# Optimization experiments

Hardware: AMD Instinct MI355X
Metric: run time of the kernel (lower is better)

Reference implementation:

```python
import jax, jax.numpy as jnp
from jax import lax
import numpy as np

B, T, IN, H, OUT = 8192, 512, 8, 64, 1


def setup_inputs() -> dict:
    key = jax.random.key(0)
    ks = jax.random.split(key, 7)
    s_ih = 1.0 / np.sqrt(H)
    # PyTorch LSTM param layout: gates stacked as [i, f, g, o] along dim 0
    W_ih = jax.random.uniform(ks[0], (4 * H, IN), jnp.float32, -s_ih, s_ih)
    W_hh = jax.random.uniform(ks[1], (4 * H, H), jnp.float32, -s_ih, s_ih)
    b_ih = jax.random.uniform(ks[2], (4 * H,), jnp.float32, -s_ih, s_ih)
    b_hh = jax.random.uniform(ks[3], (4 * H,), jnp.float32, -s_ih, s_ih)
    W_fc = jax.random.uniform(ks[4], (OUT, H), jnp.float32, -s_ih, s_ih)
    b_fc = jax.random.uniform(ks[5], (OUT,), jnp.float32, -s_ih, s_ih)
    x = jax.random.normal(ks[6], (B, T, IN), jnp.float32)
    return {"x": x, "W_ih": W_ih, "W_hh": W_hh, "b_ih": b_ih,
            "b_hh": b_hh, "W_fc": W_fc, "b_fc": b_fc}


def _lstm_last_h(x, W_ih, W_hh, b_ih, b_hh):
    # x: [B, T, IN] -> last hidden state [B, H]
    Bn = x.shape[0]
    Hn = W_hh.shape[1]
    b = b_ih + b_hh  # [4H]

    def step(carry, xt):
        h, c = carry  # [B, H] each
        gates = xt @ W_ih.T + h @ W_hh.T + b  # [B, 4H]
        i, f, g, o = jnp.split(gates, 4, axis=-1)
        i = jax.nn.sigmoid(i)
        f = jax.nn.sigmoid(f)
        g = jnp.tanh(g)
        o = jax.nn.sigmoid(o)
        c = f * c + i * g
        h = o * jnp.tanh(c)
        return (h, c), None

    h0 = jnp.zeros((Bn, Hn), x.dtype)
    c0 = jnp.zeros((Bn, Hn), x.dtype)
    (hT, _), _ = lax.scan(step, (h0, c0), jnp.swapaxes(x, 0, 1))  # scan over T
    return hT


def reference(x, W_ih, W_hh, b_ih, b_hh, W_fc, b_fc):
    hT = _lstm_last_h(x, W_ih, W_hh, b_ih, b_hh)  # [B, H]
    return hT @ W_fc.T + b_fc  # [B, OUT]
```

## Files before the change

kernel.cpp:

```cpp
#include <hip/hip_runtime.h>


typedef _Float16 f16_t;
typedef _Float16 half8 __attribute__((ext_vector_type(8)));
typedef _Float16 half4 __attribute__((ext_vector_type(4)));
typedef __fp16 fp16x2 __attribute__((ext_vector_type(2)));
typedef float floatx2 __attribute__((ext_vector_type(2)));
typedef float floatx4 __attribute__((ext_vector_type(4)));

#define Bn 8192
#define Tn 512
#define INn 8
#define Hn 64
#define BT 16
#define CHUNK 16
#define NCHUNK (Tn / CHUNK)
#define HSTRIDE 72
#define XROW 24

#define SOFT_BARRIER() asm volatile("s_waitcnt lgkmcnt(0)\n\ts_barrier" ::: "memory")

__device__ __forceinline__ floatx2 act_pair(float zi0, float zi1,
                                            float zf0, float zf1,
                                            float zg0, float zg1,
                                            float zo0, float zo1,
                                            floatx2& chat) {
  const floatx2 one  = {1.f, 1.f};
  const float  K2   = 2.8853900817779268f;
  const floatx2 K2v  = {K2, K2};
  const floatx2 mK2v = {-K2, -K2};
  const floatx2 clmp = {126.f, 126.f};
  floatx2 A = {__builtin_amdgcn_exp2f(zi0), __builtin_amdgcn_exp2f(zi1)};
  floatx2 G = {__builtin_amdgcn_exp2f(zg0), __builtin_amdgcn_exp2f(zg1)};
  floatx2 F = {__builtin_amdgcn_exp2f(zf0), __builtin_amdgcn_exp2f(zf1)};
  floatx2 O = {__builtin_amdgcn_exp2f(zo0), __builtin_amdgcn_exp2f(zo1)};
  floatx2 PA  = A + one;
  floatx2 PG  = G + one;
  floatx2 PF  = F + one;
  floatx2 PAG = PA * PG;
  floatx2 num = __builtin_elementwise_fma(G, K2v, mK2v) * PF;
  floatx2 s   = __builtin_elementwise_fma(chat, PAG, num);
  floatx2 P3  = PF * PAG;
  floatx2 R   = {__builtin_amdgcn_rcpf(P3.x), __builtin_amdgcn_rcpf(P3.y)};
  chat = __builtin_elementwise_min(s * R, clmp);
  floatx2 C2 = {__builtin_amdgcn_exp2f(chat.x), __builtin_amdgcn_exp2f(chat.y)};
  floatx2 P4 = (O + one) * (C2 + one);
  floatx2 Rh = {__builtin_amdgcn_rcpf(P4.x), __builtin_amdgcn_rcpf(P4.y)};
  return (C2 - one) * Rh;
}

__global__ __launch_bounds__(256, 2)
void lstm_fused(const float* __restrict__ xg,
                const float* __restrict__ W_ih,
                const float* __restrict__ W_hh,
                const float* __restrict__ b_ih,
                const float* __restrict__ b_hh,
                const float* __restrict__ W_fc,
                const float* __restrict__ b_fc,
                float* __restrict__ out)
{
  __shared__ alignas(16) f16_t hbuf[2][BT][HSTRIDE];
  __shared__ alignas(16) f16_t xlds[2][CHUNK][BT][XROW];

  const int tid   = threadIdx.x;
  const int wv    = tid >> 6;
  const int lane  = tid & 63;
  const int n     = lane & 15;
  const int q     = lane >> 4;
  const int bbase = blockIdx.x * BT;

  const float LOG2E = 1.4426950408889634f;

  half8 bf[4][2];
  half4 bfx[4];
  #pragma unroll
  for (int g = 0; g < 4; ++g) {
    const float sc = (g == 2) ? (2.f * LOG2E) : (-LOG2E);
    const int C = g * 64 + wv * 16 + n;
    #pragma unroll
    for (int c = 0; c < 2; ++c) {
      half8 v;
      #pragma unroll
      for (int j = 0; j < 8; ++j) {
        const int k = c * 32 + q * 8 + j;
        v[j] = (f16_t)(W_hh[C * Hn + k] * sc);
      }
      bf[g][c] = v;
    }
    half4 vx;
    #pragma unroll
    for (int j = 0; j < 4; ++j) {
      const int k = q * 4 + j;
      vx[j] = (f16_t)((k < INn) ? (W_ih[C * INn + k] * sc) : 0.f);
    }
    bfx[g] = vx;
  }

  const int u0 = wv * 16 + q * 4;
  floatx4 bi, bfv, bg, bo;
  #pragma unroll
  for (int r = 0; r < 4; ++r) {
    const int uu = u0 + r;
    bi[r]  = -(b_ih[uu]        + b_hh[uu])        * LOG2E;
    bfv[r] = -(b_ih[64 + uu]   + b_hh[64 + uu])   * LOG2E;
    bg[r]  =  (b_ih[128 + uu]  + b_hh[128 + uu])  * (2.f * LOG2E);
    bo[r]  = -(b_ih[192 + uu]  + b_hh[192 + uu])  * LOG2E;
  }

  const int row_s = tid >> 4;
  const int tt_s  = tid & 15;
  const float* xps = xg + ((size_t)(bbase + row_s) * Tn + tt_s) * INn;

  for (int i = tid; i < BT * HSTRIDE; i += 256) ((f16_t*)hbuf[0])[i] = (f16_t)0.f;
  {
    const half8 z = {};
    #pragma unroll
    for (int r = tid; r < 2 * CHUNK * BT; r += 256) {
      f16_t* base = &xlds[r >> 8][(r >> 4) & 15][r & 15][0];
      *(half8*)(base + 8)  = z;
      *(half8*)(base + 16) = z;
    }
  }
  {
    float4 a  = *(const float4*)(xps);
    float4 b2 = *(const float4*)(xps + 4);
    union { half8 v; fp16x2 h2[4]; } P;
    P.h2[0] = __builtin_amdgcn_cvt_pkrtz(a.x, a.y);
    P.h2[1] = __builtin_amdgcn_cvt_pkrtz(a.z, a.w);
    P.h2[2] = __builtin_amdgcn_cvt_pkrtz(b2.x, b2.y);
    P.h2[3] = __builtin_amdgcn_cvt_pkrtz(b2.z, b2.w);
    *(half8*)&xlds[0][tt_s][row_s][0] = P.v;
  }
  float4 pa  = *(const float4*)(xps + CHUNK * INn);
  float4 pb2 = *(const float4*)(xps + CHUNK * INn + 4);

  __syncthreads();

  if (blockIdx.x & 256) {
    #pragma unroll
    for (int sdel = 0; sdel < 6; ++sdel) __builtin_amdgcn_s_sleep(2);
  }

  floatx2 chat01 = {0.f, 0.f};
  floatx2 chat23 = {0.f, 0.f};

  for (int ch = 0; ch < NCHUNK; ++ch) {
    half4 bx[CHUNK];
    #pragma unroll
    for (int t = 0; t < CHUNK; ++t)
      bx[t] = *(const half4*)&xlds[ch & 1][t][n][q * 4];

    #pragma unroll
    for (int tt = 0; tt < CHUNK; ++tt) {
      const int p  = tt & 1;
      const int pn = p ^ 1;

      const half8 b0 = *(const half8*)&hbuf[p][n][q * 8];
      const half8 b1 = *(const half8*)&hbuf[p][n][32 + q * 8];

      __builtin_amdgcn_s_setprio(1);
      floatx4 ai = __builtin_amdgcn_mfma_f32_16x16x32_f16(bf[0][0], b0, bi,  0, 0, 0);
      floatx4 af = __builtin_amdgcn_mfma_f32_16x16x32_f16(bf[1][0], b0, bfv, 0, 0, 0);
      floatx4 ag = __builtin_amdgcn_mfma_f32_16x16x32_f16(bf[2][0], b0, bg,  0, 0, 0);
      floatx4 ao = __builtin_amdgcn_mfma_f32_16x16x32_f16(bf[3][0], b0, bo,  0, 0, 0);
      ai = __builtin_amdgcn_mfma_f32_16x16x32_f16(bf[0][1], b1, ai, 0, 0, 0);
      af = __builtin_amdgcn_mfma_f32_16x16x32_f16(bf[1][1], b1, af, 0, 0, 0);
      ag = __builtin_amdgcn_mfma_f32_16x16x32_f16(bf[2][1], b1, ag, 0, 0, 0);
      ao = __builtin_amdgcn_mfma_f32_16x16x32_f16(bf[3][1], b1, ao, 0, 0, 0);
      ai = __builtin_amdgcn_mfma_f32_16x16x16f16(bfx[0], bx[tt], ai, 0, 0, 0);
      af = __builtin_amdgcn_mfma_f32_16x16x16f16(bfx[1], bx[tt], af, 0, 0, 0);
      ag = __builtin_amdgcn_mfma_f32_16x16x16f16(bfx[2], bx[tt], ag, 0, 0, 0);
      ao = __builtin_amdgcn_mfma_f32_16x16x16f16(bfx[3], bx[tt], ao, 0, 0, 0);
      __builtin_amdgcn_s_setprio(0);

      if (tt == 0) {
        union { half8 v; fp16x2 h2[4]; } P;
        P.h2[0] = __builtin_amdgcn_cvt_pkrtz(pa.x, pa.y);
        P.h2[1] = __builtin_amdgcn_cvt_pkrtz(pa.z, pa.w);
        P.h2[2] = __builtin_amdgcn_cvt_pkrtz(pb2.x, pb2.y);
        P.h2[3] = __builtin_amdgcn_cvt_pkrtz(pb2.z, pb2.w);
        *(half8*)&xlds[(ch + 1) & 1][tt_s][row_s][0] = P.v;
      }
      if (tt == 1) {
        const int chn = (ch + 2 < NCHUNK) ? (ch + 2) : (ch + 2 - NCHUNK);
        pa  = *(const float4*)(xps + (size_t)chn * CHUNK * INn);
        pb2 = *(const float4*)(xps + (size_t)chn * CHUNK * INn + 4);
      }

      const floatx2 h01 = act_pair(ai[0], ai[1], af[0], af[1],
                                   ag[0], ag[1], ao[0], ao[1], chat01);
      const floatx2 h23 = act_pair(ai[2], ai[3], af[2], af[3],
                                   ag[2], ag[3], ao[2], ao[3], chat23);

      union { half4 v; fp16x2 h2[2]; } Wq;
      Wq.h2[0] = __builtin_amdgcn_cvt_pkrtz(h01.x, h01.y);
      Wq.h2[1] = __builtin_amdgcn_cvt_pkrtz(h23.x, h23.y);
      *(half4*)&hbuf[pn][n][u0] = Wq.v;

      SOFT_BARRIER();
    }
  }

  if (tid < 64) {
    const int b = lane & 15;
    const int part = lane >> 4;
    float s = 0.f;
    #pragma unroll
    for (int k = 0; k < 16; ++k) {
      const int uu = part * 16 + k;
      s = __builtin_fmaf((float)hbuf[0][b][uu], W_fc[uu], s);
    }
    s += __shfl_down(s, 32);
    s += __shfl_down(s, 16);
    if (lane < 16) out[bbase + b] = s + b_fc[0];
  }
}

extern "C" void kernel_launch(void* const* d_in, const int* in_sizes, int n_in,
                              void* d_out, int out_size, void* d_ws, size_t ws_size,
                              hipStream_t stream) {
  const float* x    = (const float*)d_in[0];
  const float* W_ih = (const float*)d_in[1];
  const float* W_hh = (const float*)d_in[2];
  const float* b_ih = (const float*)d_in[3];
  const float* b_hh = (const float*)d_in[4];
  const float* W_fc = (const float*)d_in[5];
  const float* b_fc = (const float*)d_in[6];
  float* out = (float*)d_out;
  dim3 grid(Bn / BT), block(256);
  hipLaunchKernelGGL(lstm_fused, grid, block, 0, stream,
                     x, W_ih, W_hh, b_ih, b_hh, W_fc, b_fc, out);
}
```

Measured before the change: 437.9 us.

## Interleave two batch tiles per block to overlap MFMA with activations

Each block now owns two 16-row batch tiles instead of one. Within each timestep it issues the gate MFMAs of one tile while computing the activations of the other, with a barrier after each half-step. This is meant to hide the dependent MFMA-to-activation latency explicitly rather than relying on two co-resident blocks per CU, so launch bounds drop to one block per CU and the grid is halved. The s_sleep stagger, setprio hints and per-chunk register caching of x are removed. In exchange there are twice as many barriers per block, extra LDS reads of x every step, and one wasted MFMA batch at the end of the loop.

```diff
diff --git a/kernel.cpp b/kernel.cpp
--- a/kernel.cpp
+++ b/kernel.cpp
@@ -13,6 +13,7 @@
 #define INn 8
 #define Hn 64
 #define BT 16
+#define NT 2
 #define CHUNK 16
 #define NCHUNK (Tn / CHUNK)
 #define HSTRIDE 72
@@ -49,7 +50,7 @@
   return (C2 - one) * Rh;
 }
 
-__global__ __launch_bounds__(256, 2)
+__global__ __launch_bounds__(256, 1)
 void lstm_fused(const float* __restrict__ xg,
                 const float* __restrict__ W_ih,
                 const float* __restrict__ W_hh,
@@ -59,15 +60,15 @@
                 const float* __restrict__ b_fc,
                 float* __restrict__ out)
 {
-  __shared__ alignas(16) f16_t hbuf[2][BT][HSTRIDE];
-  __shared__ alignas(16) f16_t xlds[2][CHUNK][BT][XROW];
+  __shared__ alignas(16) f16_t hbuf[NT][2][BT][HSTRIDE];
+  __shared__ alignas(16) f16_t xlds[NT][2][CHUNK][BT][XROW];
 
   const int tid   = threadIdx.x;
   const int wv    = tid >> 6;
   const int lane  = tid & 63;
   const int n     = lane & 15;
   const int q     = lane >> 4;
-  const int bbase = blockIdx.x * BT;
+  const int bbase = blockIdx.x * (BT * NT);
 
   const float LOG2E = 1.4426950408889634f;
 
@@ -109,110 +110,168 @@
 
   const int row_s = tid >> 4;
   const int tt_s  = tid & 15;
-  const float* xps = xg + ((size_t)(bbase + row_s) * Tn + tt_s) * INn;
-
-  for (int i = tid; i < BT * HSTRIDE; i += 256) ((f16_t*)hbuf[0])[i] = (f16_t)0.f;
+  const float* xps0 = xg + ((size_t)(bbase + row_s) * Tn + tt_s) * INn;
+  const float* xps1 = xps0 + (size_t)BT * Tn * INn;
+
+  for (int i = tid; i < NT * 2 * BT * HSTRIDE; i += 256)
+    ((f16_t*)hbuf)[i] = (f16_t)0.f;
   {
     const half8 z = {};
-    #pragma unroll
-    for (int r = tid; r < 2 * CHUNK * BT; r += 256) {
-      f16_t* base = &xlds[r >> 8][(r >> 4) & 15][r & 15][0];
+    for (int r = tid; r < NT * 2 * CHUNK * BT; r += 256) {
+      f16_t* base = ((f16_t*)xlds) + (size_t)r * XROW;
       *(half8*)(base + 8)  = z;
       *(half8*)(base + 16) = z;
     }
   }
   {
-    float4 a  = *(const float4*)(xps);
-    float4 b2 = *(const float4*)(xps + 4);
+    float4 a  = *(const float4*)(xps0);
+    float4 b2 = *(const float4*)(xps0 + 4);
     union { half8 v; fp16x2 h2[4]; } P;
     P.h2[0] = __builtin_amdgcn_cvt_pkrtz(a.x, a.y);
     P.h2[1] = __builtin_amdgcn_cvt_pkrtz(a.z, a.w);
     P.h2[2] = __builtin_amdgcn_cvt_pkrtz(b2.x, b2.y);
     P.h2[3] = __builtin_amdgcn_cvt_pkrtz(b2.z, b2.w);
-    *(half8*)&xlds[0][tt_s][row_s][0] = P.v;
-  }
-  float4 pa  = *(const float4*)(xps + CHUNK * INn);
-  float4 pb2 = *(const float4*)(xps + CHUNK * INn + 4);
+    *(half8*)&xlds[0][0][tt_s][row_s][0] = P.v;
+    a  = *(const float4*)(xps1);
+    b2 = *(const float4*)(xps1 + 4);
+    P.h2[0] = __builtin_amdgcn_cvt_pkrtz(a.x, a.y);
+    P.h2[1] = __builtin_amdgcn_cvt_pkrtz(a.z, a.w);
+    P.h2[2] = __builtin_amdgcn_cvt_pkrtz(b2.x, b2.y);
+    P.h2[3] = __builtin_amdgcn_cvt_pkrtz(b2.z, b2.w);
+    *(half8*)&xlds[1][0][tt_s][row_s][0] = P.v;
+  }
+  float4 pa0 = *(const float4*)(xps0 + CHUNK * INn);
+  float4 pb0 = *(const float4*)(xps0 + CHUNK * INn + 4);
+  float4 pa1 = *(const float4*)(xps1 + CHUNK * INn);
+  float4 pb1 = *(const float4*)(xps1 + CHUNK * INn + 4);
 
   __syncthreads();
 
-  if (blockIdx.x & 256) {
-    #pragma unroll
-    for (int sdel = 0; sdel < 6; ++sdel) __builtin_amdgcn_s_sleep(2);
-  }
-
-  floatx2 chat01 = {0.f, 0.f};
-  floatx2 chat23 = {0.f, 0.f};
+  floatx2 chat0_01 = {0.f, 0.f}, chat0_23 = {0.f, 0.f};
+  floatx2 chat1_01 = {0.f, 0.f}, chat1_23 = {0.f, 0.f};
+
+  floatx4 t0i, t0f, t0g, t0o;
+  {
+    const half8 d0 = *(const half8*)&hbuf[0][0][n][q * 8];
+    const half8 d1 = *(const half8*)&hbuf[0][0][n][32 + q * 8];
+    const half4 bx0 = *(const half4*)&xlds[0][0][0][n][q * 4];
+    t0i = __builtin_amdgcn_mfma_f32_16x16x32_f16(bf[0][0], d0, bi,  0, 0, 0);
+    t0f = __builtin_amdgcn_mfma_f32_16x16x32_f16(bf[1][0], d0, bfv, 0, 0, 0);
+    t0g = __builtin_amdgcn_mfma_f32_16x16x32_f16(bf[2][0], d0, bg,  0, 0, 0);
+    t0o = __builtin_amdgcn_mfma_f32_16x16x32_f16(bf[3][0], d0, bo,  0, 0, 0);
+    t0i = __builtin_amdgcn_mfma_f32_16x16x32_f16(bf[0][1], d1, t0i, 0, 0, 0);
+    t0f = __builtin_amdgcn_mfma_f32_16x16x32_f16(bf[1][1], d1, t0f, 0, 0, 0);
+    t0g = __builtin_amdgcn_mfma_f32_16x16x32_f16(bf[2][1], d1, t0g, 0, 0, 0);
+    t0o = __builtin_amdgcn_mfma_f32_16x16x32_f16(bf[3][1], d1, t0o, 0, 0, 0);
+    t0i = __builtin_amdgcn_mfma_f32_16x16x16f16(bfx[0], bx0, t0i, 0, 0, 0);
+    t0f = __builtin_amdgcn_mfma_f32_16x16x16f16(bfx[1], bx0, t0f, 0, 0, 0);
+    t0g = __builtin_amdgcn_mfma_f32_16x16x16f16(bfx[2], bx0, t0g, 0, 0, 0);
+    t0o = __builtin_amdgcn_mfma_f32_16x16x16f16(bfx[3], bx0, t0o, 0, 0, 0);
+  }
 
   for (int ch = 0; ch < NCHUNK; ++ch) {
-    half4 bx[CHUNK];
-    #pragma unroll
-    for (int t = 0; t < CHUNK; ++t)
-      bx[t] = *(const half4*)&xlds[ch & 1][t][n][q * 4];
-
     #pragma unroll
     for (int tt = 0; tt < CHUNK; ++tt) {
       const int p  = tt & 1;
       const int pn = p ^ 1;
-
-      const half8 b0 = *(const half8*)&hbuf[p][n][q * 8];
-      const half8 b1 = *(const half8*)&hbuf[p][n][32 + q * 8];
-
-      __builtin_amdgcn_s_setprio(1);
-      floatx4 ai = __builtin_amdgcn_mfma_f32_16x16x32_f16(bf[0][0], b0, bi,  0, 0, 0);
-      floatx4 af = __builtin_amdgcn_mfma_f32_16x16x32_f16(bf[1][0], b0, bfv, 0, 0, 0);
-      floatx4 ag = __builtin_amdgcn_mfma_f32_16x16x32_f16(bf[2][0], b0, bg,  0, 0, 0);
-      floatx4 ao = __builtin_amdgcn_mfma_f32_16x16x32_f16(bf[3][0], b0, bo,  0, 0, 0);
-      ai = __builtin_amdgcn_mfma_f32_16x16x32_f16(bf[0][1], b1, ai, 0, 0, 0);
-      af = __builtin_amdgcn_mfma_f32_16x16x32_f16(bf[1][1], b1, af, 0, 0, 0);
-      ag = __builtin_amdgcn_mfma_f32_16x16x32_f16(bf[2][1], b1, ag, 0, 0, 0);
-      ao = __builtin_amdgcn_mfma_f32_16x16x32_f16(bf[3][1], b1, ao, 0, 0, 0);
-      ai = __builtin_amdgcn_mfma_f32_16x16x16f16(bfx[0], bx[tt], ai, 0, 0, 0);
-      af = __builtin_amdgcn_mfma_f32_16x16x16f16(bfx[1], bx[tt], af, 0, 0, 0);
-      ag = __builtin_amdgcn_mfma_f32_16x16x16f16(bfx[2], bx[tt], ag, 0, 0, 0);
-      ao = __builtin_amdgcn_mfma_f32_16x16x16f16(bfx[3], bx[tt], ao, 0, 0, 0);
-      __builtin_amdgcn_s_setprio(0);
+      const int cp = ch & 1;
+
+      const half8 c0  = *(const half8*)&hbuf[1][p][n][q * 8];
+      const half8 c1  = *(const half8*)&hbuf[1][p][n][32 + q * 8];
+      const half4 bx1 = *(const half4*)&xlds[1][cp][tt][n][q * 4];
 
       if (tt == 0) {
         union { half8 v; fp16x2 h2[4]; } P;
-        P.h2[0] = __builtin_amdgcn_cvt_pkrtz(pa.x, pa.y);
-        P.h2[1] = __builtin_amdgcn_cvt_pkrtz(pa.z, pa.w);
-        P.h2[2] = __builtin_amdgcn_cvt_pkrtz(pb2.x, pb2.y);
-        P.h2[3] = __builtin_amdgcn_cvt_pkrtz(pb2.z, pb2.w);
-        *(half8*)&xlds[(ch + 1) & 1][tt_s][row_s][0] = P.v;
+        P.h2[0] = __builtin_amdgcn_cvt_pkrtz(pa0.x, pa0.y);
+        P.h2[1] = __builtin_amdgcn_cvt_pkrtz(pa0.z, pa0.w);
+        P.h2[2] = __builtin_amdgcn_cvt_pkrtz(pb0.x, pb0.y);
+        P.h2[3] = __builtin_amdgcn_cvt_pkrtz(pb0.z, pb0.w);
+        *(half8*)&xlds[0][(ch + 1) & 1][tt_s][row_s][0] = P.v;
+        P.h2[0] = __builtin_amdgcn_cvt_pkrtz(pa1.x, pa1.y);
+        P.h2[1] = __builtin_amdgcn_cvt_pkrtz(pa1.z, pa1.w);
+        P.h2[2] = __builtin_amdgcn_cvt_pkrtz(pb1.x, pb1.y);
+        P.h2[3] = __builtin_amdgcn_cvt_pkrtz(pb1.z, pb1.w);
+        *(half8*)&xlds[1][(ch + 1) & 1][tt_s][row_s][0] = P.v;
       }
       if (tt == 1) {
         const int chn = (ch + 2 < NCHUNK) ? (ch + 2) : (ch + 2 - NCHUNK);
-        pa  = *(const float4*)(xps + (size_t)chn * CHUNK * INn);
-        pb2 = *(const float4*)(xps + (size_t)chn * CHUNK * INn + 4);
-      }
-
-      const floatx2 h01 = act_pair(ai[0], ai[1], af[0], af[1],
-                                   ag[0], ag[1], ao[0], ao[1], chat01);
-      const floatx2 h23 = act_pair(ai[2], ai[3], af[2], af[3],
-                                   ag[2], ag[3], ao[2], ao[3], chat23);
-
-      union { half4 v; fp16x2 h2[2]; } Wq;
-      Wq.h2[0] = __builtin_amdgcn_cvt_pkrtz(h01.x, h01.y);
-      Wq.h2[1] = __builtin_amdgcn_cvt_pkrtz(h23.x, h23.y);
-      *(half4*)&hbuf[pn][n][u0] = Wq.v;
-
+        pa0 = *(const float4*)(xps0 + (size_t)chn * CHUNK * INn);
+        pb0 = *(const float4*)(xps0 + (size_t)chn * CHUNK * INn + 4);
+        pa1 = *(const float4*)(xps1 + (size_t)chn * CHUNK * INn);
+        pb1 = *(const float4*)(xps1 + (size_t)chn * CHUNK * INn + 4);
+      }
+
+      floatx4 u1i = __builtin_amdgcn_mfma_f32_16x16x32_f16(bf[0][0], c0, bi,  0, 0, 0);
+      floatx4 u1f = __builtin_amdgcn_mfma_f32_16x16x32_f16(bf[1][0], c0, bfv, 0, 0, 0);
+      floatx4 u1g = __builtin_amdgcn_mfma_f32_16x16x32_f16(bf[2][0], c0, bg,  0, 0, 0);
+      floatx4 u1o = __builtin_amdgcn_mfma_f32_16x16x32_f16(bf[3][0], c0, bo,  0, 0, 0);
+      u1i = __builtin_amdgcn_mfma_f32_16x16x32_f16(bf[0][1], c1, u1i, 0, 0, 0);
+      u1f = __builtin_amdgcn_mfma_f32_16x16x32_f16(bf[1][1], c1, u1f, 0, 0, 0);
+      u1g = __builtin_amdgcn_mfma_f32_16x16x32_f16(bf[2][1], c1, u1g, 0, 0, 0);
+      u1o = __builtin_amdgcn_mfma_f32_16x16x32_f16(bf[3][1], c1, u1o, 0, 0, 0);
+      u1i = __builtin_amdgcn_mfma_f32_16x16x16f16(bfx[0], bx1, u1i, 0, 0, 0);
+      u1f = __builtin_amdgcn_mfma_f32_16x16x16f16(bfx[1], bx1, u1f, 0, 0, 0);
+      u1g = __builtin_amdgcn_mfma_f32_16x16x16f16(bfx[2], bx1, u1g, 0, 0, 0);
+      u1o = __builtin_amdgcn_mfma_f32_16x16x16f16(bfx[3], bx1, u1o, 0, 0, 0);
+
+      {
+        const floatx2 h01 = act_pair(t0i[0], t0i[1], t0f[0], t0f[1],
+                                     t0g[0], t0g[1], t0o[0], t0o[1], chat0_01);
+        const floatx2 h23 = act_pair(t0i[2], t0i[3], t0f[2], t0f[3],
+                                     t0g[2], t0g[3], t0o[2], t0o[3], chat0_23);
+        union { half4 v; fp16x2 h2[2]; } Wq;
+        Wq.h2[0] = __builtin_amdgcn_cvt_pkrtz(h01.x, h01.y);
+        Wq.h2[1] = __builtin_amdgcn_cvt_pkrtz(h23.x, h23.y);
+        *(half4*)&hbuf[0][pn][n][u0] = Wq.v;
+      }
       SOFT_BARRIER();
-    }
-  }
-
-  if (tid < 64) {
+
+      const int ntt = (tt + 1) & (CHUNK - 1);
+      const int np  = (tt == CHUNK - 1) ? (cp ^ 1) : cp;
+      const half8 d0  = *(const half8*)&hbuf[0][pn][n][q * 8];
+      const half8 d1  = *(const half8*)&hbuf[0][pn][n][32 + q * 8];
+      const half4 bx0 = *(const half4*)&xlds[0][np][ntt][n][q * 4];
+
+      t0i = __builtin_amdgcn_mfma_f32_16x16x32_f16(bf[0][0], d0, bi,  0, 0, 0);
+      t0f = __builtin_amdgcn_mfma_f32_16x16x32_f16(bf[1][0], d0, bfv, 0, 0, 0);
+      t0g = __builtin_amdgcn_mfma_f32_16x16x32_f16(bf[2][0], d0, bg,  0, 0, 0);
+      t0o = __builtin_amdgcn_mfma_f32_16x16x32_f16(bf[3][0], d0, bo,  0, 0, 0);
+      t0i = __builtin_amdgcn_mfma_f32_16x16x32_f16(bf[0][1], d1, t0i, 0, 0, 0);
+      t0f = __builtin_amdgcn_mfma_f32_16x16x32_f16(bf[1][1], d1, t0f, 0, 0, 0);
+      t0g = __builtin_amdgcn_mfma_f32_16x16x32_f16(bf[2][1], d1, t0g, 0, 0, 0);
+      t0o = __builtin_amdgcn_mfma_f32_16x16x32_f16(bf[3][1], d1, t0o, 0, 0, 0);
+      t0i = __builtin_amdgcn_mfma_f32_16x16x16f16(bfx[0], bx0, t0i, 0, 0, 0);
+      t0f = __builtin_amdgcn_mfma_f32_16x16x16f16(bfx[1], bx0, t0f, 0, 0, 0);
+      t0g = __builtin_amdgcn_mfma_f32_16x16x16f16(bfx[2], bx0, t0g, 0, 0, 0);
+      t0o = __builtin_amdgcn_mfma_f32_16x16x16f16(bfx[3], bx0, t0o, 0, 0, 0);
+
+      {
+        const floatx2 h01 = act_pair(u1i[0], u1i[1], u1f[0], u1f[1],
+                                     u1g[0], u1g[1], u1o[0], u1o[1], chat1_01);
+        const floatx2 h23 = act_pair(u1i[2], u1i[3], u1f[2], u1f[3],
+                                     u1g[2], u1g[3], u1o[2], u1o[3], chat1_23);
+        union { half4 v; fp16x2 h2[2]; } Wq;
+        Wq.h2[0] = __builtin_amdgcn_cvt_pkrtz(h01.x, h01.y);
+        Wq.h2[1] = __builtin_amdgcn_cvt_pkrtz(h23.x, h23.y);
+        *(half4*)&hbuf[1][pn][n][u0] = Wq.v;
+      }
+      SOFT_BARRIER();
+    }
+  }
+
+  if (tid < 128) {
+    const int tile = wv;
     const int b = lane & 15;
     const int part = lane >> 4;
     float s = 0.f;
     #pragma unroll
     for (int k = 0; k < 16; ++k) {
       const int uu = part * 16 + k;
-      s = __builtin_fmaf((float)hbuf[0][b][uu], W_fc[uu], s);
+      s = __builtin_fmaf((float)hbuf[tile][0][b][uu], W_fc[uu], s);
     }
     s += __shfl_down(s, 32);
     s += __shfl_down(s, 16);
-    if (lane < 16) out[bbase + b] = s + b_fc[0];
+    if (lane < 16) out[bbase + tile * BT + b] = s + b_fc[0];
   }
 }
 
@@ -227,7 +286,7 @@
   const float* W_fc = (const float*)d_in[5];
   const float* b_fc = (const float*)d_in[6];
   float* out = (float*)d_out;
-  dim3 grid(Bn / BT), block(256);
+  dim3 grid(Bn / (BT * NT)), block(256);
   hipLaunchKernelGGL(lstm_fused, grid, block, 0, stream,
                      x, W_ih, W_hh, b_ih, b_hh, W_fc, b_fc, out);
 }
```

Result: slower. 526.5 us (+20.2%).
